# Kernel tuning notes

Measured on AMD Instinct MI355X. Metric: run time of the kernel, lower is better.

The kernel has to match this reference:

```python
import jax, jax.numpy as jnp
import numpy as np
jax.config.update("jax_enable_x64", True)

NUM_LAYERS = 5
WL = 5.32e-07          # wavelength
N_PIX = 128            # field grid size
PIX = 1.0e-4           # pixel size
N_NEUR = 64            # trainable phase grid size
IMG_DIST = 0.005
LAYER_DIST = 0.005
L = 3 * N_PIX          # full linear-conv size: N + (2N+1) - 1


def _prop_kernel(dist_z):
    # Rayleigh-Sommerfeld propagation kernel, (2N+1, 2N+1) complex128
    c = jnp.arange(-N_PIX, N_PIX + 1, dtype=jnp.float64) * PIX
    xg, yg = jnp.meshgrid(c, c, indexing='ij')
    r = jnp.sqrt(xg ** 2 + yg ** 2 + dist_z ** 2)
    w = (PIX ** 2) * dist_z / r ** 2 * (1.0 / (2.0 * jnp.pi * r) + 1.0 / (WL * 1j)) \
        * jnp.exp(2j * jnp.pi * r / WL)
    return w


def _kernel_fft(w):
    # torch conv2d is cross-correlation; flipping the kernel turns FFT
    # convolution into exact cross-correlation.
    return jnp.fft.fft2(w[::-1, ::-1], s=(L, L))


def _propagate(x, Wf):
    # FFT-based linear convolution, mathematically identical to
    # conv2d(x, w, padding=(N,N)): crop the central N window of the
    # full (3N) result.
    Xf = jnp.fft.fft2(x, s=(L, L))
    y = jnp.fft.ifft2(Xf * Wf)
    return y[..., N_PIX:2 * N_PIX, N_PIX:2 * N_PIX]


def _phase_mask(p):
    # constrained phase: 2*pi*sigmoid, then nearest-neighbor resize
    # N_NEUR -> N_PIX (torchvision NEAREST: src = floor(dst*in/out))
    cp = 2.0 * jnp.pi * jax.nn.sigmoid(p)
    idx = (jnp.arange(N_PIX) * N_NEUR) // N_PIX
    cp = cp[idx][:, idx]
    return jnp.exp(1j * cp.astype(jnp.float64))


def setup_inputs() -> dict:
    key = jax.random.key(0)
    k1, k2 = jax.random.split(key)
    x = jax.random.uniform(k1, (64, N_PIX, N_PIX), dtype=jnp.float32)
    # params: np.random.random - 0.5, i.e. U(-0.5, 0.5)
    phases = jax.random.uniform(k2, (NUM_LAYERS, N_NEUR, N_NEUR), dtype=jnp.float32) - 0.5
    return {"x": x, "phases": phases}


def reference(x, phases):
    Wf0 = _kernel_fft(_prop_kernel(IMG_DIST))
    Wf1 = _kernel_fft(_prop_kernel(LAYER_DIST))
    xc = x[:, None, :, :].astype(jnp.complex128)  # [B,1,N,N]
    outputs = [xc]
    for n in range(NUM_LAYERS):
        xc = _propagate(xc, Wf0 if n == 0 else Wf1)
        xc = _phase_mask(phases[n]) * xc
        outputs.append(xc)
    xc = _propagate(xc, Wf1)
    outputs.append(xc)
    x_abs = jnp.abs(xc) ** 2
    return (x_abs, *outputs)
```

## Files before the change

kernel.cpp:

```cpp
#include <hip/hip_runtime.h>
#include <math.h>

#define PI_D 3.14159265358979323846264338327950288

#define NPIX 128
#define NFFT 512
#define BATCH 64
#define EXSZ 512
#define TSTR 130

__device__ __forceinline__ float2 cmulf(float2 a, float2 b) {
    return make_float2(a.x*b.x - a.y*b.y, a.x*b.y + a.y*b.x);
}
__device__ __forceinline__ float2 cadd(float2 a, float2 b) {
    return make_float2(a.x + b.x, a.y + b.y);
}
__device__ __forceinline__ float2 csub(float2 a, float2 b) {
    return make_float2(a.x - b.x, a.y - b.y);
}

#define CBAR() __asm__ volatile("" ::: "memory")

__device__ __forceinline__ int ex1w(int k, int l)           { return 64*k  + (l ^ (2*k)); }
__device__ __forceinline__ int ex1r(int k, int k2, int hi)  { return 64*k2 + ((hi + 8*k) ^ (2*k2)); }
__device__ __forceinline__ int ex2w(int k, int l)           { return 64*k  + (l ^ (8*k)); }
__device__ __forceinline__ int ex2r(int k, int k2, int hi)  { return 64*hi + ((k2 + 8*k) ^ (8*hi)); }

template<int SGN>
__device__ __forceinline__ void dft8(float2* x)
{
    const float C = 0.70710678118654752440f;
    float2 t0 = cadd(x[0], x[4]), t4 = csub(x[0], x[4]);
    float2 t1 = cadd(x[1], x[5]), t5 = csub(x[1], x[5]);
    float2 t2 = cadd(x[2], x[6]), t6 = csub(x[2], x[6]);
    float2 t3 = cadd(x[3], x[7]), t7 = csub(x[3], x[7]);
    float2 u5 = make_float2(C*(t5.x - SGN*t5.y), C*(t5.y + SGN*t5.x));
    float2 u6 = make_float2((float)(-SGN)*t6.y, (float)SGN*t6.x);
    float2 u7 = make_float2(-C*(t7.x + SGN*t7.y), C*(SGN*t7.x - t7.y));
    float2 s0 = cadd(t0, t2), s2 = csub(t0, t2);
    float2 s1 = cadd(t1, t3), d13 = csub(t1, t3);
    float2 s3 = make_float2((float)(-SGN)*d13.y, (float)SGN*d13.x);
    x[0] = cadd(s0, s1); x[4] = csub(s0, s1);
    x[2] = cadd(s2, s3); x[6] = csub(s2, s3);
    float2 s4 = cadd(t4, u6), s6 = csub(t4, u6);
    float2 s5 = cadd(u5, u7), d57 = csub(u5, u7);
    float2 s7 = make_float2((float)(-SGN)*d57.y, (float)SGN*d57.x);
    x[1] = cadd(s4, s5); x[5] = csub(s4, s5);
    x[3] = cadd(s6, s7); x[7] = csub(s6, s7);
}

__device__ __forceinline__ void twpow(float2* x, float2 base)
{
    float2 w = base;
#pragma unroll
    for (int k = 1; k < 8; ++k) {
        x[k] = cmulf(x[k], w);
        w = cmulf(w, base);
    }
}

__device__ __forceinline__ void make_bases(int l, float2* b1, float2* b2)
{
    float s1, c1, s2, c2;
    __sincosf(0.012271846303085129838f * (float)l,        &s1, &c1);
    __sincosf(0.098174770424681038701f * (float)(l >> 3), &s2, &c2);
    *b1 = make_float2(c1, s1);
    *b2 = make_float2(c2, s2);
}

__device__ __forceinline__ void fwd512(float2* x, float2* ex, int l,
                                       float2 b1, float2 b2)
{
    const int k2 = l & 7, hi = l >> 3;
    dft8<-1>(x);
    twpow(x, b1);
    CBAR();
#pragma unroll
    for (int k = 0; k < 8; ++k) ex[ex1w(k, l)] = x[k];
    CBAR();
#pragma unroll
    for (int k = 0; k < 8; ++k) x[k] = ex[ex1r(k, k2, hi)];
    dft8<-1>(x);
    twpow(x, b2);
    CBAR();
#pragma unroll
    for (int k = 0; k < 8; ++k) ex[ex2w(k, l)] = x[k];
    CBAR();
#pragma unroll
    for (int k = 0; k < 8; ++k) x[k] = ex[ex2r(k, k2, hi)];
    dft8<-1>(x);
}

__device__ __forceinline__ void inv512(float2* x, float2* ex, int l,
                                       float2 b1, float2 b2)
{
    const int k2 = l & 7, hi = l >> 3;
    dft8<1>(x);
    CBAR();
#pragma unroll
    for (int k = 0; k < 8; ++k) ex[ex2r(k, k2, hi)] = x[k];
    CBAR();
#pragma unroll
    for (int k = 0; k < 8; ++k) x[k] = ex[ex2w(k, l)];
    twpow(x, b2);
    dft8<1>(x);
    CBAR();
#pragma unroll
    for (int k = 0; k < 8; ++k) ex[ex1r(k, k2, hi)] = x[k];
    CBAR();
#pragma unroll
    for (int k = 0; k < 8; ++k) x[k] = ex[ex1w(k, l)];
    twpow(x, b1);
    dft8<1>(x);
}

__device__ __forceinline__ int fft512d(double2 (*b)[NFFT], int t, double isign, int cur)
{
    for (int st = 0; st < 9; ++st) {
        const int s = 1 << st;
        const int p = t >> st;
        const int q = t & (s - 1);
        const int m = 256 >> st;
        const double2 a = b[cur][q + s*p];
        const double2 c = b[cur][q + s*(p + m)];
        double sw, cw;
        sincos(isign * (-PI_D/256.0) * (double)(p << st), &sw, &cw);
        const double2 dif = make_double2(a.x - c.x, a.y - c.y);
        b[cur^1][q + 2*s*p]     = make_double2(a.x + c.x, a.y + c.y);
        b[cur^1][q + 2*s*p + s] = make_double2(dif.x*cw - dif.y*sw,
                                               dif.x*sw + dif.y*cw);
        cur ^= 1;
        __syncthreads();
    }
    return cur;
}

__global__ __launch_bounds__(256) void k_build_w(double2* __restrict__ Wd)
{
    const double WLEN = 5.32e-07, PIX = 1.0e-4, DIST = 0.005;
    int idx = blockIdx.x*blockDim.x + threadIdx.x;
    int i = idx >> 9, j = idx & 511;
    double2 v = make_double2(0.0, 0.0);
    if (i < 257 && j < 257) {
        double cx = (double)(128 - i) * PIX;
        double cy = (double)(128 - j) * PIX;
        double r2 = cx*cx + cy*cy + DIST*DIST;
        double r  = sqrt(r2);
        double sc = PIX*PIX*DIST / r2;
        double re_a = 1.0/(2.0*PI_D*r);
        double im_a = -1.0/WLEN;
        double sp, cp;
        sincos(2.0*PI_D*r/WLEN, &sp, &cp);
        v.x = sc*(re_a*cp - im_a*sp);
        v.y = sc*(re_a*sp + im_a*cp);
    }
    Wd[idx] = v;
}

__global__ __launch_bounds__(256) void k_dfft_row(const double2* __restrict__ in,
                                                  double2* __restrict__ out)
{
    __shared__ double2 b[2][NFFT];
    int row = blockIdx.x, t = threadIdx.x;
    b[0][t]       = in[row*NFFT + t];
    b[0][t + 256] = in[row*NFFT + t + 256];
    __syncthreads();
    int cur = fft512d(b, t, 1.0, 0);
    out[row*NFFT + t]       = b[cur][t];
    out[row*NFFT + t + 256] = b[cur][t + 256];
}

__global__ __launch_bounds__(256) void k_dfft_col_H(const double2* __restrict__ in,
                                                    float2* __restrict__ Ht)
{
    __shared__ double2 b[2][NFFT];
    int col = blockIdx.x, t = threadIdx.x;
    b[0][t]       = in[t*NFFT + col];
    b[0][t + 256] = in[(t + 256)*NFFT + col];
    __syncthreads();
    int cur = fft512d(b, t, 1.0, 0);
    const double scale = 1.0/(512.0*512.0);
    Ht[col*NFFT + t]       = make_float2((float)(b[cur][t].x*scale),
                                         (float)(b[cur][t].y*scale));
    Ht[col*NFFT + t + 256] = make_float2((float)(b[cur][t+256].x*scale),
                                         (float)(b[cur][t+256].y*scale));
}

__global__ __launch_bounds__(256) void k_passA0(const float* __restrict__ x,
                                                float2* __restrict__ Abuf,
                                                float2* __restrict__ outc,
                                                float*  __restrict__ outr)
{
    __shared__ float2 ex_all[4*EXSZ];
    const int w = threadIdx.x >> 6, l = threadIdx.x & 63;
    const int row = blockIdx.x*4 + w, img = blockIdx.y;
    float2* ex = ex_all + w*EXSZ;
    float2 b1, b2;
    make_bases(l, &b1, &b2);

    const float* xr = x + (size_t)(img*NPIX + row)*NPIX;
    float2 v0 = make_float2(xr[l],      0.f);
    float2 v1 = make_float2(xr[l + 64], 0.f);
    size_t o = (size_t)(img*NPIX + row)*NPIX;
    if (outc) { outc[o + l] = v0; outc[o + 64 + l] = v1; }
    else      { outr[o + l] = v0.x; outr[o + 64 + l] = v1.x; }

    float2 X[8];
    X[0] = v0; X[1] = v1;
#pragma unroll
    for (int k = 2; k < 8; ++k) X[k] = make_float2(0.f, 0.f);
    fwd512(X, ex, l, make_float2(b1.x, -b1.y), make_float2(b2.x, -b2.y));
    float2* arow = Abuf + (size_t)(img*NPIX + row)*NFFT;
#pragma unroll
    for (int d = 0; d < 8; ++d) arow[l + 64*d] = X[d];
}

__global__ __launch_bounds__(512) void k_passBC(float2* __restrict__ Abuf,
                                                const float2* __restrict__ Ht)
{
    __shared__ float2 ex_all[8*EXSZ];
    float2* T = ex_all;
    const int t = threadIdx.x;
    const int w = t >> 6, l = t & 63;
    const int img = blockIdx.x, c0 = blockIdx.y*8;
    float2* base = Abuf + (size_t)img*NPIX*NFFT;
    float2 b1, b2;
    make_bases(l, &b1, &b2);

#pragma unroll
    for (int i = 0; i < 2; ++i) {
        int idx = t + 512*i;
        int cc = idx & 7, r = idx >> 3;
        T[cc*TSTR + r] = base[r*NFFT + c0 + cc];
    }
    __syncthreads();

    float2* ex = ex_all + w*EXSZ;
    float2 X[8];
    X[0] = T[w*TSTR + l];
    X[1] = T[w*TSTR + l + 64];
#pragma unroll
    for (int k = 2; k < 8; ++k) X[k] = make_float2(0.f, 0.f);
    __syncthreads();

    fwd512(X, ex, l, make_float2(b1.x, -b1.y), make_float2(b2.x, -b2.y));
    const float2* Hrow = Ht + (size_t)(c0 + w)*NFFT;
#pragma unroll
    for (int d = 0; d < 8; ++d) X[d] = cmulf(X[d], Hrow[l + 64*d]);
    inv512(X, ex, l, b1, b2);

    __syncthreads();
    T[w*TSTR + l]      = X[2];
    T[w*TSTR + l + 64] = X[3];
    __syncthreads();

#pragma unroll
    for (int i = 0; i < 2; ++i) {
        int idx = t + 512*i;
        int cc = idx & 7, r = idx >> 3;
        base[r*NFFT + c0 + cc] = T[cc*TSTR + r];
    }
}

__global__ __launch_bounds__(256) void k_passDA(float2* __restrict__ Abuf,
                                                const float* __restrict__ phases,
                                                float2* __restrict__ outc,
                                                float*  __restrict__ outr,
                                                int layer)
{
    __shared__ float2 ex_all[4*EXSZ];
    const int w = threadIdx.x >> 6, l = threadIdx.x & 63;
    const int row = blockIdx.x*4 + w, img = blockIdx.y;
    float2* ex = ex_all + w*EXSZ;
    float2 b1, b2;
    make_bases(l, &b1, &b2);

    float2* arow = Abuf + (size_t)(img*NPIX + row)*NFFT;
    float2 X[8];
#pragma unroll
    for (int d = 0; d < 8; ++d) X[d] = arow[l + 64*d];
    inv512(X, ex, l, b1, b2);

    const float* ph = phases + layer*4096 + (row >> 1)*64;
    float p0 = ph[(l >> 1)];
    float p1 = ph[32 + (l >> 1)];
    float cp0 = 6.2831853071795864769f * (1.f/(1.f + __expf(-p0)));
    float cp1 = 6.2831853071795864769f * (1.f/(1.f + __expf(-p1)));
    float s0, c0s, s1, c1s;
    __sincosf(cp0, &s0, &c0s);
    __sincosf(cp1, &s1, &c1s);
    float2 v0 = cmulf(X[2], make_float2(c0s, s0));
    float2 v1 = cmulf(X[3], make_float2(c1s, s1));

    size_t o = (size_t)(img*NPIX + row)*NPIX;
    if (outc) { outc[o + l] = v0; outc[o + 64 + l] = v1; }
    else      { outr[o + l] = v0.x; outr[o + 64 + l] = v1.x; }

    X[0] = v0; X[1] = v1;
#pragma unroll
    for (int k = 2; k < 8; ++k) X[k] = make_float2(0.f, 0.f);
    fwd512(X, ex, l, make_float2(b1.x, -b1.y), make_float2(b2.x, -b2.y));
#pragma unroll
    for (int d = 0; d < 8; ++d) arow[l + 64*d] = X[d];
}

__global__ __launch_bounds__(256) void k_passDlast(const float2* __restrict__ Abuf,
                                                   float2* __restrict__ outc,
                                                   float*  __restrict__ outr,
                                                   float*  __restrict__ outabs)
{
    __shared__ float2 ex_all[4*EXSZ];
    const int w = threadIdx.x >> 6, l = threadIdx.x & 63;
    const int row = blockIdx.x*4 + w, img = blockIdx.y;
    float2* ex = ex_all + w*EXSZ;
    float2 b1, b2;
    make_bases(l, &b1, &b2);

    const float2* arow = Abuf + (size_t)(img*NPIX + row)*NFFT;
    float2 X[8];
#pragma unroll
    for (int d = 0; d < 8; ++d) X[d] = arow[l + 64*d];
    inv512(X, ex, l, b1, b2);

    float2 v0 = X[2], v1 = X[3];
    size_t o = (size_t)(img*NPIX + row)*NPIX;
    if (outc) { outc[o + l] = v0; outc[o + 64 + l] = v1; }
    else      { outr[o + l] = v0.x; outr[o + 64 + l] = v1.x; }
    outabs[o + l]      = v0.x*v0.x + v0.y*v0.y;
    outabs[o + 64 + l] = v1.x*v1.x + v1.y*v1.y;
}

extern "C" void kernel_launch(void* const* d_in, const int* in_sizes, int n_in,
                              void* d_out, int out_size, void* d_ws, size_t ws_size,
                              hipStream_t stream)
{
    const float* x      = (const float*)d_in[0];
    const float* phases = (const float*)d_in[1];
    float* out = (float*)d_out;
    char*  ws  = (char*)d_ws;

    float2* Ht   = (float2*)ws;
    float2* Abuf = (float2*)(ws + (size_t)NFFT*NFFT*8);
    double2* Wd = (double2*)Abuf;
    double2* Td = (double2*)((char*)Abuf + (size_t)NFFT*NFFT*16);

    const bool   inter   = (out_size >= 15728640);
    const size_t cstride = inter ? 2097152u : 1048576u;

    k_build_w   <<<1024, 256, 0, stream>>>(Wd);
    k_dfft_row  <<<NFFT, 256, 0, stream>>>(Wd, Td);
    k_dfft_col_H<<<NFFT, 256, 0, stream>>>(Td, Ht);

    {
        float* c1 = out + 1048576;
        k_passA0<<<dim3(NPIX/4, BATCH), 256, 0, stream>>>(
            x, Abuf,
            inter ? (float2*)c1 : nullptr,
            inter ? nullptr : c1);
    }

    for (int step = 0; step < 6; ++step) {
        k_passBC<<<dim3(BATCH, NFFT/8), 512, 0, stream>>>(Abuf, Ht);
        float* chunk = out + 1048576 + (size_t)(step + 1)*cstride;
        if (step < 5) {
            k_passDA<<<dim3(NPIX/4, BATCH), 256, 0, stream>>>(
                Abuf, phases,
                inter ? (float2*)chunk : nullptr,
                inter ? nullptr : chunk, step);
        } else {
            k_passDlast<<<dim3(NPIX/4, BATCH), 256, 0, stream>>>(
                Abuf,
                inter ? (float2*)chunk : nullptr,
                inter ? nullptr : chunk,
                out );
        }
    }
}
```

Before: 467.9 us.

## Vectorize FFT butterflies, prune zero-input and cropped-output radix stages, precompute twiddles

Switches complex math to 2-wide ext_vector types so the compiler can emit packed FP32 ops. It adds pruned radix-8 variants: the first forward stage only combines the two nonzero inputs, and the last inverse stage only computes the two cropped outputs that are kept. The double-precision setup FFTs read a precomputed twiddle table instead of calling sincos per butterfly, and the main kernels get an occupancy hint in launch_bounds. This cuts ALU work in the bandwidth-heavy row passes, at the cost of extra specialised code paths and a workspace layout change.

After: 431.6 us. 7.7% less time.

```diff
diff --git a/kernel.cpp b/kernel.cpp
--- a/kernel.cpp
+++ b/kernel.cpp
@@ -2,6 +2,7 @@
 #include <math.h>
 
 #define PI_D 3.14159265358979323846264338327950288
+#define C707 0.70710678118654752440f
 
 #define NPIX 128
 #define NFFT 512
@@ -9,17 +10,23 @@
 #define EXSZ 512
 #define TSTR 130
 
-__device__ __forceinline__ float2 cmulf(float2 a, float2 b) {
-    return make_float2(a.x*b.x - a.y*b.y, a.x*b.y + a.y*b.x);
-}
-__device__ __forceinline__ float2 cadd(float2 a, float2 b) {
-    return make_float2(a.x + b.x, a.y + b.y);
-}
-__device__ __forceinline__ float2 csub(float2 a, float2 b) {
-    return make_float2(a.x - b.x, a.y - b.y);
-}
+typedef float v2f __attribute__((ext_vector_type(2)));
 
 #define CBAR() __asm__ volatile("" ::: "memory")
+
+__device__ __forceinline__ v2f cmul(v2f a, v2f b) {
+    v2f c; c.x = -b.y; c.y = b.x;
+    return a.xx * b + a.yy * c;
+}
+__device__ __forceinline__ v2f conjv(v2f a) {
+    v2f r; r.x = a.x; r.y = -a.y; return r;
+}
+template<int SGN> __device__ __forceinline__ v2f muli(v2f a) {
+    v2f r;
+    if (SGN > 0) { r.x = -a.y; r.y =  a.x; }
+    else         { r.x =  a.y; r.y = -a.x; }
+    return r;
+}
 
 __device__ __forceinline__ int ex1w(int k, int l)           { return 64*k  + (l ^ (2*k)); }
 __device__ __forceinline__ int ex1r(int k, int k2, int hi)  { return 64*k2 + ((hi + 8*k) ^ (2*k2)); }
@@ -27,52 +34,80 @@
 __device__ __forceinline__ int ex2r(int k, int k2, int hi)  { return 64*hi + ((k2 + 8*k) ^ (8*hi)); }
 
 template<int SGN>
-__device__ __forceinline__ void dft8(float2* x)
-{
-    const float C = 0.70710678118654752440f;
-    float2 t0 = cadd(x[0], x[4]), t4 = csub(x[0], x[4]);
-    float2 t1 = cadd(x[1], x[5]), t5 = csub(x[1], x[5]);
-    float2 t2 = cadd(x[2], x[6]), t6 = csub(x[2], x[6]);
-    float2 t3 = cadd(x[3], x[7]), t7 = csub(x[3], x[7]);
-    float2 u5 = make_float2(C*(t5.x - SGN*t5.y), C*(t5.y + SGN*t5.x));
-    float2 u6 = make_float2((float)(-SGN)*t6.y, (float)SGN*t6.x);
-    float2 u7 = make_float2(-C*(t7.x + SGN*t7.y), C*(SGN*t7.x - t7.y));
-    float2 s0 = cadd(t0, t2), s2 = csub(t0, t2);
-    float2 s1 = cadd(t1, t3), d13 = csub(t1, t3);
-    float2 s3 = make_float2((float)(-SGN)*d13.y, (float)SGN*d13.x);
-    x[0] = cadd(s0, s1); x[4] = csub(s0, s1);
-    x[2] = cadd(s2, s3); x[6] = csub(s2, s3);
-    float2 s4 = cadd(t4, u6), s6 = csub(t4, u6);
-    float2 s5 = cadd(u5, u7), d57 = csub(u5, u7);
-    float2 s7 = make_float2((float)(-SGN)*d57.y, (float)SGN*d57.x);
-    x[1] = cadd(s4, s5); x[5] = csub(s4, s5);
-    x[3] = cadd(s6, s7); x[7] = csub(s6, s7);
-}
-
-__device__ __forceinline__ void twpow(float2* x, float2 base)
-{
-    float2 w = base;
-#pragma unroll
-    for (int k = 1; k < 8; ++k) {
-        x[k] = cmulf(x[k], w);
-        w = cmulf(w, base);
-    }
-}
-
-__device__ __forceinline__ void make_bases(int l, float2* b1, float2* b2)
+__device__ __forceinline__ void dft8(v2f* x)
+{
+    v2f t0 = x[0] + x[4], t4 = x[0] - x[4];
+    v2f t1 = x[1] + x[5], t5 = x[1] - x[5];
+    v2f t2 = x[2] + x[6], t6 = x[2] - x[6];
+    v2f t3 = x[3] + x[7], t7 = x[3] - x[7];
+    v2f u5 = C707 * (t5 + muli<SGN>(t5));
+    v2f u6 = muli<SGN>(t6);
+    v2f u7 = C707 * (muli<SGN>(t7) - t7);
+    v2f s0 = t0 + t2, s2 = t0 - t2;
+    v2f s1 = t1 + t3, d13 = t1 - t3;
+    v2f s3 = muli<SGN>(d13);
+    x[0] = s0 + s1; x[4] = s0 - s1;
+    x[2] = s2 + s3; x[6] = s2 - s3;
+    v2f s4 = t4 + u6, s6 = t4 - u6;
+    v2f s5 = u5 + u7, d57 = u5 - u7;
+    v2f s7 = muli<SGN>(d57);
+    x[1] = s4 + s5; x[5] = s4 - s5;
+    x[3] = s6 + s7; x[7] = s6 - s7;
+}
+
+__device__ __forceinline__ void dft8_f2(v2f* x)
+{
+    v2f a = x[0], b = x[1];
+    v2f bw1 = C707 * (b + muli<-1>(b));
+    v2f bw2 = muli<-1>(b);
+    v2f bw3 = muli<-1>(bw1);
+    x[0] = a + b;   x[4] = a - b;
+    x[1] = a + bw1; x[5] = a - bw1;
+    x[2] = a + bw2; x[6] = a - bw2;
+    x[3] = a + bw3; x[7] = a - bw3;
+}
+
+__device__ __forceinline__ void dft8_i23(const v2f* x, v2f* o2, v2f* o3)
+{
+    v2f t0 = x[0] + x[4], t4 = x[0] - x[4];
+    v2f t1 = x[1] + x[5], t5 = x[1] - x[5];
+    v2f t2 = x[2] + x[6], t6 = x[2] - x[6];
+    v2f t3 = x[3] + x[7], t7 = x[3] - x[7];
+    v2f s2  = t0 - t2;
+    v2f d13 = t1 - t3;
+    *o2 = s2 + muli<1>(d13);
+    v2f u5 = C707 * (t5 + muli<1>(t5));
+    v2f u6 = muli<1>(t6);
+    v2f u7 = C707 * (muli<1>(t7) - t7);
+    v2f s6  = t4 - u6;
+    v2f d57 = u5 - u7;
+    *o3 = s6 + muli<1>(d57);
+}
+
+__device__ __forceinline__ void twpow(v2f* x, v2f base)
+{
+    v2f w = base;
+    x[1] = cmul(x[1], w);
+#pragma unroll
+    for (int k = 2; k < 8; ++k) {
+        w = cmul(w, base);
+        x[k] = cmul(x[k], w);
+    }
+}
+
+__device__ __forceinline__ void make_bases(int l, v2f* b1, v2f* b2)
 {
     float s1, c1, s2, c2;
     __sincosf(0.012271846303085129838f * (float)l,        &s1, &c1);
     __sincosf(0.098174770424681038701f * (float)(l >> 3), &s2, &c2);
-    *b1 = make_float2(c1, s1);
-    *b2 = make_float2(c2, s2);
-}
-
-__device__ __forceinline__ void fwd512(float2* x, float2* ex, int l,
-                                       float2 b1, float2 b2)
+    b1->x = c1; b1->y = s1;
+    b2->x = c2; b2->y = s2;
+}
+
+__device__ __forceinline__ void fwd512(v2f* x, v2f* ex, int l, v2f b1, v2f b2)
 {
     const int k2 = l & 7, hi = l >> 3;
-    dft8<-1>(x);
+    dft8_f2(x);
     twpow(x, b1);
     CBAR();
 #pragma unroll
@@ -91,8 +126,8 @@
     dft8<-1>(x);
 }
 
-__device__ __forceinline__ void inv512(float2* x, float2* ex, int l,
-                                       float2 b1, float2 b2)
+__device__ __forceinline__ void inv512_crop(v2f* x, v2f* ex, int l,
+                                            v2f b1, v2f b2, v2f* o2, v2f* o3)
 {
     const int k2 = l & 7, hi = l >> 3;
     dft8<1>(x);
@@ -111,10 +146,19 @@
 #pragma unroll
     for (int k = 0; k < 8; ++k) x[k] = ex[ex1w(k, l)];
     twpow(x, b1);
-    dft8<1>(x);
-}
-
-__device__ __forceinline__ int fft512d(double2 (*b)[NFFT], int t, double isign, int cur)
+    dft8_i23(x, o2, o3);
+}
+
+__global__ __launch_bounds__(256) void k_dtw(double2* __restrict__ dtw)
+{
+    int t = threadIdx.x;
+    double s, c;
+    sincos(-PI_D/256.0 * (double)t, &s, &c);
+    dtw[t] = make_double2(c, s);
+}
+
+__device__ __forceinline__ int fft512d(double2 (*b)[NFFT], int t, int cur,
+                                       const double2* __restrict__ tw)
 {
     for (int st = 0; st < 9; ++st) {
         const int s = 1 << st;
@@ -123,12 +167,11 @@
         const int m = 256 >> st;
         const double2 a = b[cur][q + s*p];
         const double2 c = b[cur][q + s*(p + m)];
-        double sw, cw;
-        sincos(isign * (-PI_D/256.0) * (double)(p << st), &sw, &cw);
+        const double2 wv = tw[p << st];
         const double2 dif = make_double2(a.x - c.x, a.y - c.y);
         b[cur^1][q + 2*s*p]     = make_double2(a.x + c.x, a.y + c.y);
-        b[cur^1][q + 2*s*p + s] = make_double2(dif.x*cw - dif.y*sw,
-                                               dif.x*sw + dif.y*cw);
+        b[cur^1][q + 2*s*p + s] = make_double2(dif.x*wv.x - dif.y*wv.y,
+                                               dif.x*wv.y + dif.y*wv.x);
         cur ^= 1;
         __syncthreads();
     }
@@ -158,27 +201,29 @@
 }
 
 __global__ __launch_bounds__(256) void k_dfft_row(const double2* __restrict__ in,
-                                                  double2* __restrict__ out)
+                                                  double2* __restrict__ out,
+                                                  const double2* __restrict__ tw)
 {
     __shared__ double2 b[2][NFFT];
     int row = blockIdx.x, t = threadIdx.x;
     b[0][t]       = in[row*NFFT + t];
     b[0][t + 256] = in[row*NFFT + t + 256];
     __syncthreads();
-    int cur = fft512d(b, t, 1.0, 0);
+    int cur = fft512d(b, t, 0, tw);
     out[row*NFFT + t]       = b[cur][t];
     out[row*NFFT + t + 256] = b[cur][t + 256];
 }
 
 __global__ __launch_bounds__(256) void k_dfft_col_H(const double2* __restrict__ in,
-                                                    float2* __restrict__ Ht)
+                                                    float2* __restrict__ Ht,
+                                                    const double2* __restrict__ tw)
 {
     __shared__ double2 b[2][NFFT];
     int col = blockIdx.x, t = threadIdx.x;
     b[0][t]       = in[t*NFFT + col];
     b[0][t + 256] = in[(t + 256)*NFFT + col];
     __syncthreads();
-    int cur = fft512d(b, t, 1.0, 0);
+    int cur = fft512d(b, t, 0, tw);
     const double scale = 1.0/(512.0*512.0);
     Ht[col*NFFT + t]       = make_float2((float)(b[cur][t].x*scale),
                                          (float)(b[cur][t].y*scale));
@@ -186,45 +231,43 @@
                                          (float)(b[cur][t+256].y*scale));
 }
 
-__global__ __launch_bounds__(256) void k_passA0(const float* __restrict__ x,
-                                                float2* __restrict__ Abuf,
-                                                float2* __restrict__ outc,
-                                                float*  __restrict__ outr)
-{
-    __shared__ float2 ex_all[4*EXSZ];
+__global__ __launch_bounds__(256, 8) void k_passA0(const float* __restrict__ x,
+                                                   v2f* __restrict__ Abuf,
+                                                   v2f* __restrict__ outc,
+                                                   float* __restrict__ outr)
+{
+    __shared__ v2f ex_all[4*EXSZ];
     const int w = threadIdx.x >> 6, l = threadIdx.x & 63;
     const int row = blockIdx.x*4 + w, img = blockIdx.y;
-    float2* ex = ex_all + w*EXSZ;
-    float2 b1, b2;
+    v2f* ex = ex_all + w*EXSZ;
+    v2f b1, b2;
     make_bases(l, &b1, &b2);
 
     const float* xr = x + (size_t)(img*NPIX + row)*NPIX;
-    float2 v0 = make_float2(xr[l],      0.f);
-    float2 v1 = make_float2(xr[l + 64], 0.f);
+    v2f v0; v0.x = xr[l];      v0.y = 0.f;
+    v2f v1; v1.x = xr[l + 64]; v1.y = 0.f;
     size_t o = (size_t)(img*NPIX + row)*NPIX;
     if (outc) { outc[o + l] = v0; outc[o + 64 + l] = v1; }
     else      { outr[o + l] = v0.x; outr[o + 64 + l] = v1.x; }
 
-    float2 X[8];
+    v2f X[8];
     X[0] = v0; X[1] = v1;
-#pragma unroll
-    for (int k = 2; k < 8; ++k) X[k] = make_float2(0.f, 0.f);
-    fwd512(X, ex, l, make_float2(b1.x, -b1.y), make_float2(b2.x, -b2.y));
-    float2* arow = Abuf + (size_t)(img*NPIX + row)*NFFT;
+    fwd512(X, ex, l, conjv(b1), conjv(b2));
+    v2f* arow = Abuf + (size_t)(img*NPIX + row)*NFFT;
 #pragma unroll
     for (int d = 0; d < 8; ++d) arow[l + 64*d] = X[d];
 }
 
-__global__ __launch_bounds__(512) void k_passBC(float2* __restrict__ Abuf,
-                                                const float2* __restrict__ Ht)
-{
-    __shared__ float2 ex_all[8*EXSZ];
-    float2* T = ex_all;
+__global__ __launch_bounds__(512, 8) void k_passBC(v2f* __restrict__ Abuf,
+                                                   const v2f* __restrict__ Ht)
+{
+    __shared__ v2f ex_all[8*EXSZ];
+    v2f* T = ex_all;
     const int t = threadIdx.x;
     const int w = t >> 6, l = t & 63;
     const int img = blockIdx.x, c0 = blockIdx.y*8;
-    float2* base = Abuf + (size_t)img*NPIX*NFFT;
-    float2 b1, b2;
+    v2f* base = Abuf + (size_t)img*NPIX*NFFT;
+    v2f b1, b2;
     make_bases(l, &b1, &b2);
 
 #pragma unroll
@@ -235,23 +278,22 @@
     }
     __syncthreads();
 
-    float2* ex = ex_all + w*EXSZ;
-    float2 X[8];
+    v2f* ex = ex_all + w*EXSZ;
+    v2f X[8];
     X[0] = T[w*TSTR + l];
     X[1] = T[w*TSTR + l + 64];
-#pragma unroll
-    for (int k = 2; k < 8; ++k) X[k] = make_float2(0.f, 0.f);
-    __syncthreads();
-
-    fwd512(X, ex, l, make_float2(b1.x, -b1.y), make_float2(b2.x, -b2.y));
-    const float2* Hrow = Ht + (size_t)(c0 + w)*NFFT;
-#pragma unroll
-    for (int d = 0; d < 8; ++d) X[d] = cmulf(X[d], Hrow[l + 64*d]);
-    inv512(X, ex, l, b1, b2);
-
-    __syncthreads();
-    T[w*TSTR + l]      = X[2];
-    T[w*TSTR + l + 64] = X[3];
+    __syncthreads();
+
+    fwd512(X, ex, l, conjv(b1), conjv(b2));
+    const v2f* Hrow = Ht + (size_t)(c0 + w)*NFFT;
+#pragma unroll
+    for (int d = 0; d < 8; ++d) X[d] = cmul(X[d], Hrow[l + 64*d]);
+    v2f y2, y3;
+    inv512_crop(X, ex, l, b1, b2, &y2, &y3);
+
+    __syncthreads();
+    T[w*TSTR + l]      = y2;
+    T[w*TSTR + l + 64] = y3;
     __syncthreads();
 
 #pragma unroll
@@ -262,24 +304,25 @@
     }
 }
 
-__global__ __launch_bounds__(256) void k_passDA(float2* __restrict__ Abuf,
-                                                const float* __restrict__ phases,
-                                                float2* __restrict__ outc,
-                                                float*  __restrict__ outr,
-                                                int layer)
-{
-    __shared__ float2 ex_all[4*EXSZ];
+__global__ __launch_bounds__(256, 8) void k_passDA(v2f* __restrict__ Abuf,
+                                                   const float* __restrict__ phases,
+                                                   v2f* __restrict__ outc,
+                                                   float* __restrict__ outr,
+                                                   int layer)
+{
+    __shared__ v2f ex_all[4*EXSZ];
     const int w = threadIdx.x >> 6, l = threadIdx.x & 63;
     const int row = blockIdx.x*4 + w, img = blockIdx.y;
-    float2* ex = ex_all + w*EXSZ;
-    float2 b1, b2;
+    v2f* ex = ex_all + w*EXSZ;
+    v2f b1, b2;
     make_bases(l, &b1, &b2);
 
-    float2* arow = Abuf + (size_t)(img*NPIX + row)*NFFT;
-    float2 X[8];
+    v2f* arow = Abuf + (size_t)(img*NPIX + row)*NFFT;
+    v2f X[8];
 #pragma unroll
     for (int d = 0; d < 8; ++d) X[d] = arow[l + 64*d];
-    inv512(X, ex, l, b1, b2);
+    v2f y2, y3;
+    inv512_crop(X, ex, l, b1, b2, &y2, &y3);
 
     const float* ph = phases + layer*4096 + (row >> 1)*64;
     float p0 = ph[(l >> 1)];
@@ -289,40 +332,40 @@
     float s0, c0s, s1, c1s;
     __sincosf(cp0, &s0, &c0s);
     __sincosf(cp1, &s1, &c1s);
-    float2 v0 = cmulf(X[2], make_float2(c0s, s0));
-    float2 v1 = cmulf(X[3], make_float2(c1s, s1));
+    v2f m0; m0.x = c0s; m0.y = s0;
+    v2f m1; m1.x = c1s; m1.y = s1;
+    v2f v0 = cmul(y2, m0);
+    v2f v1 = cmul(y3, m1);
 
     size_t o = (size_t)(img*NPIX + row)*NPIX;
     if (outc) { outc[o + l] = v0; outc[o + 64 + l] = v1; }
     else      { outr[o + l] = v0.x; outr[o + 64 + l] = v1.x; }
 
     X[0] = v0; X[1] = v1;
-#pragma unroll
-    for (int k = 2; k < 8; ++k) X[k] = make_float2(0.f, 0.f);
-    fwd512(X, ex, l, make_float2(b1.x, -b1.y), make_float2(b2.x, -b2.y));
+    fwd512(X, ex, l, conjv(b1), conjv(b2));
 #pragma unroll
     for (int d = 0; d < 8; ++d) arow[l + 64*d] = X[d];
 }
 
-__global__ __launch_bounds__(256) void k_passDlast(const float2* __restrict__ Abuf,
-                                                   float2* __restrict__ outc,
-                                                   float*  __restrict__ outr,
-                                                   float*  __restrict__ outabs)
-{
-    __shared__ float2 ex_all[4*EXSZ];
+__global__ __launch_bounds__(256, 8) void k_passDlast(const v2f* __restrict__ Abuf,
+                                                      v2f* __restrict__ outc,
+                                                      float* __restrict__ outr,
+                                                      float* __restrict__ outabs)
+{
+    __shared__ v2f ex_all[4*EXSZ];
     const int w = threadIdx.x >> 6, l = threadIdx.x & 63;
     const int row = blockIdx.x*4 + w, img = blockIdx.y;
-    float2* ex = ex_all + w*EXSZ;
-    float2 b1, b2;
+    v2f* ex = ex_all + w*EXSZ;
+    v2f b1, b2;
     make_bases(l, &b1, &b2);
 
-    const float2* arow = Abuf + (size_t)(img*NPIX + row)*NFFT;
-    float2 X[8];
+    const v2f* arow = Abuf + (size_t)(img*NPIX + row)*NFFT;
+    v2f X[8];
 #pragma unroll
     for (int d = 0; d < 8; ++d) X[d] = arow[l + 64*d];
-    inv512(X, ex, l, b1, b2);
-
-    float2 v0 = X[2], v1 = X[3];
+    v2f v0, v1;
+    inv512_crop(X, ex, l, b1, b2, &v0, &v1);
+
     size_t o = (size_t)(img*NPIX + row)*NPIX;
     if (outc) { outc[o + l] = v0; outc[o + 64 + l] = v1; }
     else      { outr[o + l] = v0.x; outr[o + 64 + l] = v1.x; }
@@ -339,38 +382,40 @@
     float* out = (float*)d_out;
     char*  ws  = (char*)d_ws;
 
-    float2* Ht   = (float2*)ws;
-    float2* Abuf = (float2*)(ws + (size_t)NFFT*NFFT*8);
+    float2*  HtF  = (float2*)ws;
+    double2* dtw  = (double2*)(ws + (size_t)NFFT*NFFT*8);
+    v2f*     Abuf = (v2f*)(ws + (size_t)NFFT*NFFT*8 + 4096);
     double2* Wd = (double2*)Abuf;
     double2* Td = (double2*)((char*)Abuf + (size_t)NFFT*NFFT*16);
 
     const bool   inter   = (out_size >= 15728640);
     const size_t cstride = inter ? 2097152u : 1048576u;
 
+    k_dtw       <<<1,    256, 0, stream>>>(dtw);
     k_build_w   <<<1024, 256, 0, stream>>>(Wd);
-    k_dfft_row  <<<NFFT, 256, 0, stream>>>(Wd, Td);
-    k_dfft_col_H<<<NFFT, 256, 0, stream>>>(Td, Ht);
+    k_dfft_row  <<<NFFT, 256, 0, stream>>>(Wd, Td, dtw);
+    k_dfft_col_H<<<NFFT, 256, 0, stream>>>(Td, HtF, dtw);
 
     {
         float* c1 = out + 1048576;
         k_passA0<<<dim3(NPIX/4, BATCH), 256, 0, stream>>>(
             x, Abuf,
-            inter ? (float2*)c1 : nullptr,
+            inter ? (v2f*)c1 : nullptr,
             inter ? nullptr : c1);
     }
 
     for (int step = 0; step < 6; ++step) {
-        k_passBC<<<dim3(BATCH, NFFT/8), 512, 0, stream>>>(Abuf, Ht);
+        k_passBC<<<dim3(BATCH, NFFT/8), 512, 0, stream>>>(Abuf, (const v2f*)HtF);
         float* chunk = out + 1048576 + (size_t)(step + 1)*cstride;
         if (step < 5) {
             k_passDA<<<dim3(NPIX/4, BATCH), 256, 0, stream>>>(
                 Abuf, phases,
-                inter ? (float2*)chunk : nullptr,
+                inter ? (v2f*)chunk : nullptr,
                 inter ? nullptr : chunk, step);
         } else {
             k_passDlast<<<dim3(NPIX/4, BATCH), 256, 0, stream>>>(
                 Abuf,
-                inter ? (float2*)chunk : nullptr,
+                inter ? (v2f*)chunk : nullptr,
                 inter ? nullptr : chunk,
                 out );
         }
```
